# Optimization experiments

Hardware: AMD Instinct MI355X
Metric: run time of the kernel (lower is better)

## Reference

```python
import jax, jax.numpy as jnp
import numpy as np

B, S, E, H, M = 4, 2048, 1024, 16, 32  # batch, seq, hidden, heads, max_rel_dist
D = E // H  # head dim


def setup_inputs() -> dict:
    key = jax.random.key(0)
    ks = jax.random.split(key, 4)
    x = jax.random.normal(ks[0], (B, S, E), dtype=jnp.float32)
    in_proj_w = jax.random.normal(ks[1], (3 * E, E), dtype=jnp.float32) * (E ** -0.5)
    in_proj_b = jnp.zeros((3 * E,), dtype=jnp.float32)
    out_w = jax.random.normal(ks[2], (E, E), dtype=jnp.float32) * (E ** -0.5)
    out_b = jnp.zeros((E,), dtype=jnp.float32)
    rel_bias = jax.random.normal(ks[3], (2 * M + 1, H), dtype=jnp.float32) * 0.02
    return {"x": x, "in_proj_w": in_proj_w, "in_proj_b": in_proj_b,
            "out_w": out_w, "out_b": out_b, "rel_bias": rel_bias}


def reference(x, in_proj_w, in_proj_b, out_w, out_b, rel_bias):
    b, s, e = x.shape
    # relative position index: clamp(i-j, -M, M) + M  -> [S, S]
    rel_pos = jnp.clip(jnp.arange(s)[:, None] - jnp.arange(s)[None, :], -M, M) + M
    # gather per-head bias then average over heads (matches the per-head sum / H loop)
    attn_mask = rel_bias[rel_pos].mean(axis=-1)  # [S, S]

    # fused QKV projection (torch in_proj: x @ W^T + b)
    qkv = x @ in_proj_w.T + in_proj_b  # [B, S, 3E]
    q, k, v = jnp.split(qkv, 3, axis=-1)
    # reshape to heads: [B, H, S, D]
    q = q.reshape(b, s, H, D).transpose(0, 2, 1, 3)
    k = k.reshape(b, s, H, D).transpose(0, 2, 1, 3)
    v = v.reshape(b, s, H, D).transpose(0, 2, 1, 3)

    scores = jnp.einsum("bhqd,bhkd->bhqk", q, k) * (D ** -0.5) + attn_mask
    attn = jax.nn.softmax(scores, axis=-1)
    out = jnp.einsum("bhqk,bhkd->bhqd", attn, v)  # [B, H, S, D]
    out = out.transpose(0, 2, 1, 3).reshape(b, s, e)
    return out @ out_w.T + out_b
```

## Files before the change

kernel.cpp:

```cpp
#include <hip/hip_runtime.h>
#include <hip/hip_fp16.h>
#include <stdint.h>
#include <stddef.h>


typedef _Float16 half8 __attribute__((ext_vector_type(8)));
typedef _Float16 half2v __attribute__((ext_vector_type(2)));
typedef float f32x4 __attribute__((ext_vector_type(4)));
typedef float f32x16 __attribute__((ext_vector_type(16)));
typedef uint32_t u32x4 __attribute__((ext_vector_type(4)));

#define MFMA16(a, b, c) __builtin_amdgcn_mfma_f32_16x16x32_f16(a, b, c, 0, 0, 0)
#define MFMA32(a, b, c) __builtin_amdgcn_mfma_f32_32x32x16_f16(a, b, c, 0, 0, 0)

__device__ static inline void gload_lds16(const void* g, void* l) {
  __builtin_amdgcn_global_load_lds(
      (const __attribute__((address_space(1))) void*)g,
      (__attribute__((address_space(3))) void*)l, 16, 0, 0);
}

__device__ static inline uint32_t pkhalf(float a, float b) {
  half2v p; p[0] = (_Float16)a; p[1] = (_Float16)b;
  return __builtin_bit_cast(uint32_t, p);
}

__global__ void cvt_f32_f16(const float* __restrict__ in, __half* __restrict__ out,
                            int n8) {
  int i = blockIdx.x * blockDim.x + threadIdx.x;
  int stride = gridDim.x * blockDim.x;
  for (; i < n8; i += stride) {
    const float4* p = (const float4*)in + (size_t)i * 2;
    float4 a = p[0], b = p[1];
    half8 h;
    h[0] = (_Float16)a.x; h[1] = (_Float16)a.y; h[2] = (_Float16)a.z; h[3] = (_Float16)a.w;
    h[4] = (_Float16)b.x; h[5] = (_Float16)b.y; h[6] = (_Float16)b.z; h[7] = (_Float16)b.w;
    *(half8*)(out + (size_t)i * 8) = h;
  }
}

__global__ void bias_mean_kernel(const float* __restrict__ rb, float* __restrict__ mb) {
  int r = threadIdx.x;
  if (r < 65) {
    float s = 0.f;
    #pragma unroll
    for (int h = 0; h < 16; ++h) s += rb[r * 16 + h];
    mb[r] = s * (1.44269504f / 16.f);
  }
}

template <bool OUT_HALF>
__global__ __launch_bounds__(256)
void gemm_bt(const __half* __restrict__ A, const __half* __restrict__ Bm,
             const float* __restrict__ bias, void* __restrict__ Cout,
             int Ndim, int K) {
  __shared__ __align__(16) __half As[128 * 32];
  __shared__ __align__(16) __half Bs[128 * 32];
  const int tid = threadIdx.x;
  const int lane = tid & 63;
  const int wave = tid >> 6;
  const int wr = wave >> 1, wc = wave & 1;
  const int bm = blockIdx.y, bn = blockIdx.x;
  const int l15 = lane & 15;
  const int kseg = lane >> 4;

  f32x4 acc[4][4];
  #pragma unroll
  for (int i = 0; i < 4; ++i)
    #pragma unroll
    for (int j = 0; j < 4; ++j) {
      acc[i][j][0] = 0.f; acc[i][j][1] = 0.f; acc[i][j][2] = 0.f; acc[i][j][3] = 0.f;
    }

  const int nk = K >> 5;
  for (int kt = 0; kt < nk; ++kt) {
    __syncthreads();
    #pragma unroll
    for (int c = 0; c < 2; ++c) {
      const int off = c * 4096 + tid * 16;
      const int mloc = off >> 6;
      const int kb = off & 63;
      gload_lds16(A + (size_t)(bm * 128 + mloc) * K + kt * 32 + (kb >> 1),
                  (char*)As + c * 4096 + wave * 1024);
      gload_lds16(Bm + (size_t)(bn * 128 + mloc) * K + kt * 32 + (kb >> 1),
                  (char*)Bs + c * 4096 + wave * 1024);
    }
    __syncthreads();
    half8 af[4], bf[4];
    #pragma unroll
    for (int i = 0; i < 4; ++i) {
      af[i] = *(const half8*)&As[(wr * 64 + i * 16 + l15) * 32 + kseg * 8];
      bf[i] = *(const half8*)&Bs[(wc * 64 + i * 16 + l15) * 32 + kseg * 8];
    }
    #pragma unroll
    for (int i = 0; i < 4; ++i)
      #pragma unroll
      for (int j = 0; j < 4; ++j)
        acc[i][j] = MFMA16(af[i], bf[j], acc[i][j]);
  }

  const int crow0 = bm * 128 + wr * 64;
  const int ccol0 = bn * 128 + wc * 64;
  #pragma unroll
  for (int j = 0; j < 4; ++j) {
    const int c = ccol0 + j * 16 + l15;
    const float bv = bias[c];
    #pragma unroll
    for (int i = 0; i < 4; ++i) {
      #pragma unroll
      for (int r = 0; r < 4; ++r) {
        const int row = crow0 + i * 16 + kseg * 4 + r;
        const float v = acc[i][j][r] + bv;
        if (OUT_HALF)
          ((__half*)Cout)[(size_t)row * Ndim + c] = __float2half_rn(v);
        else
          ((float*)Cout)[(size_t)row * Ndim + c] = v;
      }
    }
  }
}

#define MAKE_AP(pe, cp, ap_out) do {                                        \
    uint32_t QA0_ = pkhalf(pe[8*(cp)+0], pe[8*(cp)+1]);                     \
    uint32_t QA1_ = pkhalf(pe[8*(cp)+2], pe[8*(cp)+3]);                     \
    uint32_t QB0_ = pkhalf(pe[8*(cp)+4], pe[8*(cp)+5]);                     \
    uint32_t QB1_ = pkhalf(pe[8*(cp)+6], pe[8*(cp)+7]);                     \
    auto r0_ = __builtin_amdgcn_permlane32_swap(QA0_, QB0_, false, false);  \
    auto r1_ = __builtin_amdgcn_permlane32_swap(QA1_, QB1_, false, false);  \
    u32x4 uv_;                                                              \
    uv_[0] = r0_[0]; uv_[1] = r1_[0]; uv_[2] = r0_[1]; uv_[3] = r1_[1];     \
    ap_out = __builtin_bit_cast(half8, uv_);                                \
  } while (0)

#define SOFTMAX_TILE(sv, pe, tt) do {                                       \
    const int base_ = qw - kb - 32 * (tt);                                  \
    if (base_ >= 63) {                                                      \
      _Pragma("unroll")                                                     \
      for (int r_ = 0; r_ < 16; ++r_)                                       \
        pe[r_] = __builtin_amdgcn_exp2f(fmaf(sv[r_], kscale, mbs_hi));      \
    } else if (base_ <= -63) {                                              \
      _Pragma("unroll")                                                     \
      for (int r_ = 0; r_ < 16; ++r_)                                       \
        pe[r_] = __builtin_amdgcn_exp2f(fmaf(sv[r_], kscale, mbs_lo));      \
    } else {                                                                \
      _Pragma("unroll")                                                     \
      for (int r_ = 0; r_ < 16; ++r_) {                                     \
        int d_ = qs - (kb + 32 * (tt) + (r_ & 3) + 8 * (r_ >> 2) + 4 * hi); \
        d_ = min(max(d_, -32), 32);                                         \
        pe[r_] = __builtin_amdgcn_exp2f(fmaf(sv[r_], kscale, mbs[d_ + 32]));\
      }                                                                     \
    }                                                                       \
    _Pragma("unroll")                                                       \
    for (int r_ = 0; r_ < 16; ++r_) lp += pe[r_];                           \
  } while (0)

__global__ __launch_bounds__(256)
void attn_kernel(const __half* __restrict__ qkv, const float* __restrict__ mb,
                 __half* __restrict__ attn_out) {
  __shared__ __align__(16) __half Ks[2][64 * 64];
  __shared__ __align__(16) __half Vts[2][64 * 64];
  __shared__ float lshare[4][32];
  __shared__ float mbs[65];

  const int tid = threadIdx.x;
  const int lane = tid & 63;
  const int w = tid >> 6;
  const int l31 = lane & 31;
  const int hi = lane >> 5;
  const int bh = blockIdx.y;
  const int b = bh >> 4, h = bh & 15;
  const int qw = blockIdx.x * 128 + w * 32;
  const int qs = qw + l31;
  const float kscale = 0.125f * 1.44269504f;
  const int swzv = (l31 & 7) << 4;

  if (tid < 65) mbs[tid] = mb[tid];
  const float mbs_lo = mb[0];
  const float mbs_hi = mb[64];

  const size_t qrow = (size_t)(b * 2048 + qs) * 3072;
  half8 bq[4];
  #pragma unroll
  for (int s = 0; s < 4; ++s)
    bq[s] = *(const half8*)&qkv[qrow + h * 64 + s * 16 + hi * 8];

  const int krow0 = tid >> 3;
  const int kcolsw = ((tid & 7) * 16) ^ ((krow0 & 7) << 4);
  const __half* kp0 = qkv + (size_t)(b * 2048 + krow0) * 3072 + 1024 + h * 64 + (kcolsw >> 1);
  const __half* kp1 = kp0 + (size_t)32 * 3072;

  const int vk0 = (tid & 31) * 2;
  const int vds = (tid >> 5) * 8;
  const __half* vp = qkv + (size_t)(b * 2048 + vk0) * 3072 + 2048 + h * 64 + vds;

  const size_t kvstep = (size_t)64 * 3072;

  float lp = 0.f;
  f32x16 o0, o1;
  #pragma unroll
  for (int i = 0; i < 16; ++i) { o0[i] = 0.f; o1[i] = 0.f; }

  gload_lds16(kp0, (char*)Ks[0] + w * 1024);
  gload_lds16(kp1, (char*)Ks[0] + w * 1024 + 4096);
  half8 vn0 = *(const half8*)vp;
  half8 vn1 = *(const half8*)(vp + 3072);
  #pragma unroll
  for (int e = 0; e < 8; ++e) {
    half2v pr; pr[0] = vn0[e]; pr[1] = vn1[e];
    *(half2v*)((char*)Vts[0] + (vds + e) * 128 + ((vk0 * 2) ^ (e << 4))) = pr;
  }
  vn0 = *(const half8*)(vp + kvstep);
  vn1 = *(const half8*)(vp + kvstep + 3072);

  for (int kt = 0; kt < 32; ++kt) {
    const int pb = kt & 1;
    const int kb = kt * 64;
    __syncthreads();

    if (kt < 31) {
      const size_t adv = (size_t)(kt + 1) * kvstep;
      char* kdst = (char*)Ks[pb ^ 1] + w * 1024;
      gload_lds16(kp0 + adv, kdst);
      gload_lds16(kp1 + adv, kdst + 4096);
      #pragma unroll
      for (int e = 0; e < 8; ++e) {
        half2v pr; pr[0] = vn0[e]; pr[1] = vn1[e];
        *(half2v*)((char*)Vts[pb ^ 1] + (vds + e) * 128 + ((vk0 * 2) ^ (e << 4))) = pr;
      }
      if (kt < 30) {
        const size_t adv2 = (size_t)(kt + 2) * kvstep;
        vn0 = *(const half8*)(vp + adv2);
        vn1 = *(const half8*)(vp + adv2 + 3072);
      }
    }

    const char* ksb = (const char*)Ks[pb];
    f32x16 s0, s1;
    #pragma unroll
    for (int i = 0; i < 16; ++i) { s0[i] = 0.f; s1[i] = 0.f; }
    #pragma unroll
    for (int s = 0; s < 4; ++s) {
      const int cby = (s * 32 + hi * 16) ^ swzv;
      half8 ak0 = *(const half8*)(ksb + l31 * 128 + cby);
      half8 ak1 = *(const half8*)(ksb + (32 + l31) * 128 + cby);
      s0 = MFMA32(ak0, bq[s], s0);
      s1 = MFMA32(ak1, bq[s], s1);
    }

    float pe0[16], pe1[16];
    SOFTMAX_TILE(s0, pe0, 0);
    SOFTMAX_TILE(s1, pe1, 1);

    const char* vtb = (const char*)Vts[pb];
    half8 ap;
    #pragma unroll
    for (int c = 0; c < 4; ++c) {
      if (c == 0)      MAKE_AP(pe0, 0, ap);
      else if (c == 1) MAKE_AP(pe0, 1, ap);
      else if (c == 2) MAKE_AP(pe1, 0, ap);
      else             MAKE_AP(pe1, 1, ap);
      const int cby = (32 * c + 16 * hi) ^ swzv;
      half8 bv0 = *(const half8*)(vtb + l31 * 128 + cby);
      half8 bv1 = *(const half8*)(vtb + (32 + l31) * 128 + cby);
      o0 = MFMA32(ap, bv0, o0);
      o1 = MFMA32(ap, bv1, o1);
    }
  }

  lp += __shfl_xor(lp, 32, 64);
  if (hi == 0) lshare[w][l31] = lp;
  #pragma unroll
  for (int r = 0; r < 16; ++r) {
    const int ql = (r & 3) + 8 * (r >> 2) + 4 * hi;
    const float rl = 1.f / lshare[w][ql];
    const size_t row = (size_t)(b * 2048 + qw + ql) * 1024 + h * 64;
    attn_out[row + l31]      = __float2half(o0[r] * rl);
    attn_out[row + 32 + l31] = __float2half(o1[r] * rl);
  }
}

extern "C" void kernel_launch(void* const* d_in, const int* in_sizes, int n_in,
                              void* d_out, int out_size, void* d_ws, size_t ws_size,
                              hipStream_t stream) {
  const float* x    = (const float*)d_in[0];
  const float* in_w = (const float*)d_in[1];
  const float* in_b = (const float*)d_in[2];
  const float* ow   = (const float*)d_in[3];
  const float* ob   = (const float*)d_in[4];
  const float* rb   = (const float*)d_in[5];

  char* ws = (char*)d_ws;
  __half* xh   = (__half*)(ws);
  __half* wh   = (__half*)(ws + 16777216);
  __half* owh  = (__half*)(ws + 23068672);
  float*  mb   = (float*)(ws + 25165824);
  __half* qkvh = (__half*)(ws + 25166336);
  __half* atth = (__half*)(ws + 75497984);

  cvt_f32_f16<<<2048, 256, 0, stream>>>(x, xh, (8192 * 1024) / 8);
  cvt_f32_f16<<<1536, 256, 0, stream>>>(in_w, wh, (3072 * 1024) / 8);
  cvt_f32_f16<<<512, 256, 0, stream>>>(ow, owh, (1024 * 1024) / 8);
  bias_mean_kernel<<<1, 128, 0, stream>>>(rb, mb);

  gemm_bt<true><<<dim3(24, 64), 256, 0, stream>>>(xh, wh, in_b, qkvh, 3072, 1024);
  attn_kernel<<<dim3(16, 64), 256, 0, stream>>>(qkvh, mb, atth);
  gemm_bt<false><<<dim3(8, 64), 256, 0, stream>>>(atth, owh, ob, (float*)d_out, 1024, 1024);
}
```

Measured before the change: 248.9 us.

## Fuse conversion kernels, remap attention blocks, add MFMA priority and occupancy hint

Merges the three fp32-to-fp16 conversions and the bias-mean computation into one launch, which cuts per-launch overhead. In the attention kernel, blocks are remapped so that neighbouring workgroups spread across different (batch, head) pairs, launch bounds now request 5 blocks per CU, and s_setprio is raised around the MFMA sections. The LDS bias table and the lshare array are removed: the bias is read from global memory and the row sums reuse the K buffer. Reading bias from global on the diagonal tiles could add latency, and the lshare alias relies on no pending reads of Ks at that point.

```diff
diff --git a/kernel.cpp b/kernel.cpp
--- a/kernel.cpp
+++ b/kernel.cpp
@@ -24,27 +24,31 @@
   return __builtin_bit_cast(uint32_t, p);
 }
 
-__global__ void cvt_f32_f16(const float* __restrict__ in, __half* __restrict__ out,
-                            int n8) {
+__global__ void cvt_all(const float* __restrict__ x, const float* __restrict__ w,
+                        const float* __restrict__ ow, const float* __restrict__ rb,
+                        __half* __restrict__ xh, __half* __restrict__ wh,
+                        __half* __restrict__ owh, float* __restrict__ mbg,
+                        int nx, int nw, int no) {
+  if (blockIdx.x == 0 && threadIdx.x < 65) {
+    float s = 0.f;
+    #pragma unroll
+    for (int hh = 0; hh < 16; ++hh) s += rb[threadIdx.x * 16 + hh];
+    mbg[threadIdx.x] = s * (1.44269504f / 16.f);
+  }
+  const int total = nx + nw + no;
   int i = blockIdx.x * blockDim.x + threadIdx.x;
-  int stride = gridDim.x * blockDim.x;
-  for (; i < n8; i += stride) {
-    const float4* p = (const float4*)in + (size_t)i * 2;
+  const int stride = gridDim.x * blockDim.x;
+  for (; i < total; i += stride) {
+    const float* src; __half* dst; int j;
+    if (i < nx)            { src = x;  dst = xh;  j = i; }
+    else if (i < nx + nw)  { src = w;  dst = wh;  j = i - nx; }
+    else                   { src = ow; dst = owh; j = i - nx - nw; }
+    const float4* p = (const float4*)src + (size_t)j * 2;
     float4 a = p[0], b = p[1];
-    half8 h;
-    h[0] = (_Float16)a.x; h[1] = (_Float16)a.y; h[2] = (_Float16)a.z; h[3] = (_Float16)a.w;
-    h[4] = (_Float16)b.x; h[5] = (_Float16)b.y; h[6] = (_Float16)b.z; h[7] = (_Float16)b.w;
-    *(half8*)(out + (size_t)i * 8) = h;
-  }
-}
-
-__global__ void bias_mean_kernel(const float* __restrict__ rb, float* __restrict__ mb) {
-  int r = threadIdx.x;
-  if (r < 65) {
-    float s = 0.f;
-    #pragma unroll
-    for (int h = 0; h < 16; ++h) s += rb[r * 16 + h];
-    mb[r] = s * (1.44269504f / 16.f);
+    half8 hv;
+    hv[0] = (_Float16)a.x; hv[1] = (_Float16)a.y; hv[2] = (_Float16)a.z; hv[3] = (_Float16)a.w;
+    hv[4] = (_Float16)b.x; hv[5] = (_Float16)b.y; hv[6] = (_Float16)b.z; hv[7] = (_Float16)b.w;
+    *(half8*)(dst + (size_t)j * 8) = hv;
   }
 }
 
@@ -146,34 +150,33 @@
       for (int r_ = 0; r_ < 16; ++r_) {                                     \
         int d_ = qs - (kb + 32 * (tt) + (r_ & 3) + 8 * (r_ >> 2) + 4 * hi); \
         d_ = min(max(d_, -32), 32);                                         \
-        pe[r_] = __builtin_amdgcn_exp2f(fmaf(sv[r_], kscale, mbs[d_ + 32]));\
+        pe[r_] = __builtin_amdgcn_exp2f(fmaf(sv[r_], kscale, mb[d_ + 32])); \
       }                                                                     \
     }                                                                       \
     _Pragma("unroll")                                                       \
     for (int r_ = 0; r_ < 16; ++r_) lp += pe[r_];                           \
   } while (0)
 
-__global__ __launch_bounds__(256)
+__global__ __launch_bounds__(256, 5)
 void attn_kernel(const __half* __restrict__ qkv, const float* __restrict__ mb,
                  __half* __restrict__ attn_out) {
   __shared__ __align__(16) __half Ks[2][64 * 64];
   __shared__ __align__(16) __half Vts[2][64 * 64];
-  __shared__ float lshare[4][32];
-  __shared__ float mbs[65];
 
   const int tid = threadIdx.x;
   const int lane = tid & 63;
   const int w = tid >> 6;
   const int l31 = lane & 31;
   const int hi = lane >> 5;
-  const int bh = blockIdx.y;
+  const int flat = (blockIdx.y << 4) | blockIdx.x;
+  const int nid = (flat & 7) * 128 + (flat >> 3);
+  const int bh = nid >> 4;
   const int b = bh >> 4, h = bh & 15;
-  const int qw = blockIdx.x * 128 + w * 32;
+  const int qw = (nid & 15) * 128 + w * 32;
   const int qs = qw + l31;
   const float kscale = 0.125f * 1.44269504f;
   const int swzv = (l31 & 7) << 4;
 
-  if (tid < 65) mbs[tid] = mb[tid];
   const float mbs_lo = mb[0];
   const float mbs_hi = mb[64];
 
@@ -237,6 +240,7 @@
     f32x16 s0, s1;
     #pragma unroll
     for (int i = 0; i < 16; ++i) { s0[i] = 0.f; s1[i] = 0.f; }
+    __builtin_amdgcn_s_setprio(1);
     #pragma unroll
     for (int s = 0; s < 4; ++s) {
       const int cby = (s * 32 + hi * 16) ^ swzv;
@@ -245,6 +249,7 @@
       s0 = MFMA32(ak0, bq[s], s0);
       s1 = MFMA32(ak1, bq[s], s1);
     }
+    __builtin_amdgcn_s_setprio(0);
 
     float pe0[16], pe1[16];
     SOFTMAX_TILE(s0, pe0, 0);
@@ -252,6 +257,7 @@
 
     const char* vtb = (const char*)Vts[pb];
     half8 ap;
+    __builtin_amdgcn_s_setprio(1);
     #pragma unroll
     for (int c = 0; c < 4; ++c) {
       if (c == 0)      MAKE_AP(pe0, 0, ap);
@@ -264,14 +270,16 @@
       o0 = MFMA32(ap, bv0, o0);
       o1 = MFMA32(ap, bv1, o1);
     }
+    __builtin_amdgcn_s_setprio(0);
   }
 
   lp += __shfl_xor(lp, 32, 64);
-  if (hi == 0) lshare[w][l31] = lp;
+  float* lsh = ((float*)Ks) + w * 32;
+  if (hi == 0) lsh[l31] = lp;
   #pragma unroll
   for (int r = 0; r < 16; ++r) {
     const int ql = (r & 3) + 8 * (r >> 2) + 4 * hi;
-    const float rl = 1.f / lshare[w][ql];
+    const float rl = 1.f / lsh[ql];
     const size_t row = (size_t)(b * 2048 + qw + ql) * 1024 + h * 64;
     attn_out[row + l31]      = __float2half(o0[r] * rl);
     attn_out[row + 32 + l31] = __float2half(o1[r] * rl);
@@ -296,10 +304,9 @@
   __half* qkvh = (__half*)(ws + 25166336);
   __half* atth = (__half*)(ws + 75497984);
 
-  cvt_f32_f16<<<2048, 256, 0, stream>>>(x, xh, (8192 * 1024) / 8);
-  cvt_f32_f16<<<1536, 256, 0, stream>>>(in_w, wh, (3072 * 1024) / 8);
-  cvt_f32_f16<<<512, 256, 0, stream>>>(ow, owh, (1024 * 1024) / 8);
-  bias_mean_kernel<<<1, 128, 0, stream>>>(rb, mb);
+  cvt_all<<<2048, 256, 0, stream>>>(x, in_w, ow, rb, xh, wh, owh, mb,
+                                    (8192 * 1024) / 8, (3072 * 1024) / 8,
+                                    (1024 * 1024) / 8);
 
   gemm_bt<true><<<dim3(24, 64), 256, 0, stream>>>(xh, wh, in_b, qkvh, 3072, 1024);
   attn_kernel<<<dim3(16, 64), 256, 0, stream>>>(qkvh, mb, atth);
```

Measured after the change: 374.7 us. +50.5%, slower.
